# Performance work log

Measured on AMD Instinct MI355X. Metric: run time of the kernel, lower is better.

## Reference

```python
import jax, jax.numpy as jnp
import numpy as np

B, N, DIM = 16, 1024, 512
H, DH = 8, 64
INNER = H * DH            # 512
FF = 4 * DIM              # 2048
CIN = 2 * DIM             # conv inner dim = dim*expansion_factor = 1024
K = 31                    # depthwise kernel size
MAXPOS = 512
EPS = 1e-5


def layernorm(x, g, b):
    mu = jnp.mean(x, axis=-1, keepdims=True)
    var = jnp.mean(jnp.square(x - mu), axis=-1, keepdims=True)
    return (x - mu) * jax.lax.rsqrt(var + EPS) * g + b


def swish(x):
    return x * jax.nn.sigmoid(x)


def feed_forward(x, w1, b1, w2, b2):
    h = swish(x @ w1 + b1)
    return h @ w2 + b2


def setup_inputs() -> dict:
    key = jax.random.key(0)
    ks = jax.random.split(key, 16)
    s = 0.02
    w = lambda k, shape: (jax.random.normal(k, shape, jnp.float32) * s)
    inp = {
        "x": jax.random.normal(ks[0], (B, N, DIM), jnp.float32),
        # FF1
        "ff1_ln_g": jnp.ones((DIM,), jnp.float32), "ff1_ln_b": jnp.zeros((DIM,), jnp.float32),
        "ff1_w1": w(ks[1], (DIM, FF)), "ff1_b1": jnp.zeros((FF,), jnp.float32),
        "ff1_w2": w(ks[2], (FF, DIM)), "ff1_b2": jnp.zeros((DIM,), jnp.float32),
        # Attention (PreNorm)
        "attn_ln_g": jnp.ones((DIM,), jnp.float32), "attn_ln_b": jnp.zeros((DIM,), jnp.float32),
        "wq": w(ks[3], (DIM, INNER)),
        "wkv": w(ks[4], (DIM, 2 * INNER)),
        "wo": w(ks[5], (INNER, DIM)), "bo": jnp.zeros((DIM,), jnp.float32),
        "rel_emb": w(ks[6], (2 * MAXPOS + 1, DH)),
        # Conv module
        "conv_ln_g": jnp.ones((DIM,), jnp.float32), "conv_ln_b": jnp.zeros((DIM,), jnp.float32),
        "conv1_w": w(ks[7], (DIM, 2 * CIN)), "conv1_b": jnp.zeros((2 * CIN,), jnp.float32),
        "dw_w": w(ks[8], (CIN, 1, K)), "dw_b": jnp.zeros((CIN,), jnp.float32),
        "conv2_w": w(ks[9], (CIN, DIM)), "conv2_b": jnp.zeros((DIM,), jnp.float32),
        # FF2
        "ff2_ln_g": jnp.ones((DIM,), jnp.float32), "ff2_ln_b": jnp.zeros((DIM,), jnp.float32),
        "ff2_w1": w(ks[10], (DIM, FF)), "ff2_b1": jnp.zeros((FF,), jnp.float32),
        "ff2_w2": w(ks[11], (FF, DIM)), "ff2_b2": jnp.zeros((DIM,), jnp.float32),
        # post norm
        "post_ln_g": jnp.ones((DIM,), jnp.float32), "post_ln_b": jnp.zeros((DIM,), jnp.float32),
    }
    return inp


def attention(x, wq, wkv, wo, bo, rel_emb):
    b, n, _ = x.shape
    scale = DH ** -0.5
    q = (x @ wq).reshape(b, n, H, DH).transpose(0, 2, 1, 3)   # b h n d
    kv = x @ wkv
    k = kv[..., :INNER].reshape(b, n, H, DH).transpose(0, 2, 1, 3)
    v = kv[..., INNER:].reshape(b, n, H, DH).transpose(0, 2, 1, 3)
    dots = jnp.einsum("bhid,bhjd->bhij", q, k) * scale
    # relative positional bias via embedding lookup
    seq = jnp.arange(n)
    dist = jnp.clip(seq[:, None] - seq[None, :], -MAXPOS, MAXPOS) + MAXPOS  # [n, n]
    rel = jnp.take(rel_emb, dist, axis=0)                      # [n, n, d]
    pos = jnp.einsum("bhnd,njd->bhnj", q, rel) * scale
    attn = jax.nn.softmax(dots + pos, axis=-1)
    out = jnp.einsum("bhij,bhjd->bhid", attn, v)
    out = out.transpose(0, 2, 1, 3).reshape(b, n, INNER)
    return out @ wo + bo


def conv_module(x, ln_g, ln_b, conv1_w, conv1_b, dw_w, dw_b, conv2_w, conv2_b):
    h = layernorm(x, ln_g, ln_b)                               # [b, n, dim]
    h = h @ conv1_w + conv1_b                                  # pointwise conv -> [b, n, 2*CIN]
    a, g = h[..., :CIN], h[..., CIN:]
    h = a * jax.nn.sigmoid(g)                                  # GLU (channel dim)
    hc = h.transpose(0, 2, 1)                                  # [b, CIN, n]
    hc = jnp.pad(hc, ((0, 0), (0, 0), (K - 1, 0)))             # causal left pad
    hc = jax.lax.conv_general_dilated(
        hc, dw_w, window_strides=(1,), padding="VALID",
        feature_group_count=CIN, dimension_numbers=("NCH", "OIH", "NCH"),
    ) + dw_b[None, :, None]
    h = hc.transpose(0, 2, 1)                                  # [b, n, CIN]
    h = swish(h)
    return h @ conv2_w + conv2_b


def reference(x, ff1_ln_g, ff1_ln_b, ff1_w1, ff1_b1, ff1_w2, ff1_b2,
              attn_ln_g, attn_ln_b, wq, wkv, wo, bo, rel_emb,
              conv_ln_g, conv_ln_b, conv1_w, conv1_b, dw_w, dw_b, conv2_w, conv2_b,
              ff2_ln_g, ff2_ln_b, ff2_w1, ff2_b1, ff2_w2, ff2_b2,
              post_ln_g, post_ln_b):
    x = 0.5 * feed_forward(layernorm(x, ff1_ln_g, ff1_ln_b), ff1_w1, ff1_b1, ff1_w2, ff1_b2) + x
    x = attention(layernorm(x, attn_ln_g, attn_ln_b), wq, wkv, wo, bo, rel_emb) + x
    x = conv_module(x, conv_ln_g, conv_ln_b, conv1_w, conv1_b, dw_w, dw_b, conv2_w, conv2_b) + x
    x = 0.5 * feed_forward(layernorm(x, ff2_ln_g, ff2_ln_b), ff2_w1, ff2_b1, ff2_w2, ff2_b2) + x
    return layernorm(x, post_ln_g, post_ln_b)
```

## Files before the change

### kernel.cpp

```cpp
#include <hip/hip_runtime.h>


#define BN 16384

typedef unsigned short u16;
typedef __attribute__((ext_vector_type(8))) __bf16 bf16x8;
typedef __attribute__((ext_vector_type(4))) float f32x4;
typedef __attribute__((ext_vector_type(8))) unsigned short u16x8;

__device__ __forceinline__ float sigf(float x) { return 1.f / (1.f + __expf(-x)); }
__device__ __forceinline__ u16 f2bf(float f) {
  unsigned int u = __float_as_uint(f);
  u += 0x7FFF + ((u >> 16) & 1);
  return (u16)(u >> 16);
}
__device__ __forceinline__ float bf2f(u16 u) {
  return __uint_as_float(((unsigned int)u) << 16);
}
__device__ __forceinline__ void gl_lds16(const void* g, void* lds) {
  __builtin_amdgcn_global_load_lds(
      (const __attribute__((address_space(1))) unsigned int*)g,
      (__attribute__((address_space(3))) unsigned int*)lds, 16, 0, 0);
}

__global__ __launch_bounds__(256) void ln_kernel(const float* __restrict__ in,
    const float* __restrict__ g, const float* __restrict__ b,
    u16* outb, float* outf) {
  const int row = blockIdx.x;
  const int t = threadIdx.x;
  const float2 v = ((const float2*)(in + (size_t)row * 512))[t];
  float s = v.x + v.y;
  float sq = v.x * v.x + v.y * v.y;
#pragma unroll
  for (int o = 32; o > 0; o >>= 1) {
    s += __shfl_down(s, o);
    sq += __shfl_down(sq, o);
  }
  __shared__ float ss[4], ssq[4];
  if ((t & 63) == 0) { ss[t >> 6] = s; ssq[t >> 6] = sq; }
  __syncthreads();
  s = ss[0] + ss[1] + ss[2] + ss[3];
  sq = ssq[0] + ssq[1] + ssq[2] + ssq[3];
  const float mu = s * (1.f / 512.f);
  const float var = fmaxf(sq * (1.f / 512.f) - mu * mu, 0.f);
  const float rstd = rsqrtf(var + 1e-5f);
  const float2 gg = ((const float2*)g)[t];
  const float2 bb = ((const float2*)b)[t];
  float ox = (v.x - mu) * rstd * gg.x + bb.x;
  float oy = (v.y - mu) * rstd * gg.y + bb.y;
  if (outf) {
    float2 o2 = {ox, oy};
    ((float2*)(outf + (size_t)row * 512))[t] = o2;
  } else {
    ushort2 u2 = {f2bf(ox), f2bf(oy)};
    ((ushort2*)(outb + (size_t)row * 512))[t] = u2;
  }
}

__global__ __launch_bounds__(256) void wtrans(const float* __restrict__ W,
                                              u16* __restrict__ WT, int K, int N) {
  const int n0 = blockIdx.x * 32, k0 = blockIdx.y * 32;
  const int t = threadIdx.x;
  const int tx = t & 31, ty = t >> 5;
  __shared__ float T[32][33];
#pragma unroll
  for (int i = 0; i < 4; ++i)
    T[tx][ty + 8 * i] = W[(size_t)(k0 + ty + 8 * i) * N + n0 + tx];
  __syncthreads();
#pragma unroll
  for (int i = 0; i < 4; ++i)
    WT[(size_t)(n0 + ty + 8 * i) * K + k0 + tx] = f2bf(T[ty + 8 * i][tx]);
}

__global__ __launch_bounds__(256) void cvt_bf16(const float* __restrict__ in,
                                                u16* __restrict__ out, int n) {
  const int i = blockIdx.x * 256 + threadIdx.x;
  if (i < n) out[i] = f2bf(in[i]);
}

__global__ __launch_bounds__(256) void gemm_bf16(const u16* __restrict__ A,
    const u16* __restrict__ WT, const float* __restrict__ bias,
    const float* res, float* Cf, u16* Cb, u16* VTout, int K, int N, int ldc,
    float alpha, int act) {
  __shared__ __align__(16) u16 Ast[128 * 32];
  __shared__ __align__(16) u16 Bst[128 * 32];
  const int t = threadIdx.x;
  int bx = blockIdx.x, by = blockIdx.y;
  {
    const int nx = gridDim.x;
    const int lin = bx + nx * by;
    const int xcd = lin & 7;
    const int s = lin >> 3;
    const int ny8 = gridDim.y >> 3;
    const int sy = s / nx;
    by = xcd * ny8 + sy;
    bx = s - sy * nx;
  }
  const int n0 = bx * 128;
  const int m0 = by * 128;
  const int w = t >> 6;
  const int lc = t & 15, lq = (t >> 4) & 3;
  const int wy = w >> 1, wx = w & 1;
  f32x4 acc[4][4];
#pragma unroll
  for (int i = 0; i < 4; ++i)
#pragma unroll
    for (int j = 0; j < 4; ++j)
#pragma unroll
      for (int r = 0; r < 4; ++r) acc[i][j][r] = 0.f;

  for (int kt = 0; kt < K; kt += 32) {
#pragma unroll
    for (int s = 0; s < 2; ++s) {
      const int f = t + 256 * s;
      gl_lds16(&A[(size_t)(m0 + (f >> 2)) * K + kt + (f & 3) * 8], &Ast[f * 8]);
      gl_lds16(&WT[(size_t)(n0 + (f >> 2)) * K + kt + (f & 3) * 8], &Bst[f * 8]);
    }
    __syncthreads();
    bf16x8 bfr[4];
#pragma unroll
    for (int j = 0; j < 4; ++j)
      bfr[j] = *(const bf16x8*)&Bst[(wx * 64 + j * 16 + lc) * 32 + lq * 8];
#pragma unroll
    for (int i = 0; i < 4; ++i) {
      const bf16x8 af = *(const bf16x8*)&Ast[(wy * 64 + i * 16 + lc) * 32 + lq * 8];
#pragma unroll
      for (int j = 0; j < 4; ++j)
        acc[i][j] = __builtin_amdgcn_mfma_f32_16x16x32_bf16(af, bfr[j], acc[i][j], 0, 0, 0);
    }
    __syncthreads();
  }

#pragma unroll
  for (int j = 0; j < 4; ++j) {
    const int col = n0 + wx * 64 + j * 16 + lc;
    const float bj = bias ? bias[col] : 0.f;
    const bool vtc = (VTout != nullptr) && (col >= 512);
#pragma unroll
    for (int i = 0; i < 4; ++i) {
      const int row0 = m0 + wy * 64 + i * 16 + lq * 4;
      float v4[4];
#pragma unroll
      for (int r = 0; r < 4; ++r) {
        float v = acc[i][j][r] + bj;
        if (act) v = v * sigf(v);
        v *= alpha;
        if (res) v += res[(size_t)(row0 + r) * ldc + col];
        v4[r] = v;
      }
      if (vtc) {
        const int cm = col - 512;
        const int hh = cm >> 6, dd = cm & 63;
        const int bb = row0 >> 10, nl = row0 & 1023;
        ushort4 o4 = {f2bf(v4[0]), f2bf(v4[1]), f2bf(v4[2]), f2bf(v4[3])};
        *(ushort4*)&VTout[((size_t)((bb * 8 + hh) * 64 + dd)) * 1024 + nl] = o4;
      } else {
#pragma unroll
        for (int r = 0; r < 4; ++r) {
          const size_t off = (size_t)(row0 + r) * ldc + col;
          if (Cf) Cf[off] = v4[r];
          else Cb[off] = f2bf(v4[r]);
        }
      }
    }
  }
}

__global__ __launch_bounds__(256) void attn_mfma(const u16* __restrict__ QKV,
    const u16* __restrict__ Vt, const u16* __restrict__ Rb, u16* __restrict__ O) {
  const int lin = blockIdx.x;
  const int hb = lin & 127;
  const int n0 = (lin >> 7) * 64;
  const int h = hb & 7, b = hb >> 3;
  const int t = threadIdx.x;
  const int w = t >> 6;
  const int lc = t & 15, lq = (t >> 4) & 3;

  __shared__ __align__(16) u16 Ks[64 * 72];
  __shared__ __align__(16) u16 Vs[64 * 72];
  __shared__ __align__(16) u16 SP[64 * 72];

  bf16x8 qf[2];
  {
    const size_t qrow = (size_t)(b * 1024 + n0 + w * 16 + lc) * 1536 + h * 64;
    qf[0] = *(const bf16x8*)&QKV[qrow + lq * 8];
    qf[1] = *(const bf16x8*)&QKV[qrow + 32 + lq * 8];
  }

  float l_r[4] = {0.f, 0.f, 0.f, 0.f};
  f32x4 o[4];
#pragma unroll
  for (int dt = 0; dt < 4; ++dt)
#pragma unroll
    for (int r = 0; r < 4; ++r) o[dt][r] = 0.f;

  for (int jt = 0; jt < 16; ++jt) {
    const int j0 = jt * 64;
#pragma unroll
    for (int s = 0; s < 2; ++s) {
      const int f = t + 256 * s;
      const int row = f >> 3, c8 = (f & 7) * 8;
      const u16x8 kv =
          *(const u16x8*)&QKV[(size_t)(b * 1024 + j0 + row) * 1536 + 512 + h * 64 + c8];
      const u16x8 vv =
          *(const u16x8*)&Vt[(size_t)((b * 8 + h) * 64 + row) * 1024 + j0 + c8];
      *(u16x8*)&Ks[row * 72 + c8] = kv;
      *(u16x8*)&Vs[row * 72 + c8] = vv;
    }
    __syncthreads();

    f32x4 qk[4], pa[5];
#pragma unroll
    for (int j = 0; j < 4; ++j)
#pragma unroll
      for (int r = 0; r < 4; ++r) qk[j][r] = 0.f;
#pragma unroll
    for (int rtl = 0; rtl < 5; ++rtl)
#pragma unroll
      for (int r = 0; r < 4; ++r) pa[rtl][r] = 0.f;

    const int base = n0 - j0 - 63;
#pragma unroll
    for (int ks = 0; ks < 2; ++ks) {
      bf16x8 rfr[5];
#pragma unroll
      for (int rtl = 0; rtl < 5; ++rtl) {
        const int didx = (w + rtl) * 16 + lc;
        int p = base + didx;
        p = (p < -512 ? -512 : (p > 512 ? 512 : p)) + 512;
        rfr[rtl] = *(const bf16x8*)&Rb[(size_t)p * 64 + ks * 32 + lq * 8];
      }
#pragma unroll
      for (int j = 0; j < 4; ++j) {
        const bf16x8 bf = *(const bf16x8*)&Ks[(j * 16 + lc) * 72 + ks * 32 + lq * 8];
        qk[j] = __builtin_amdgcn_mfma_f32_16x16x32_bf16(qf[ks], bf, qk[j], 0, 0, 0);
      }
#pragma unroll
      for (int rtl = 0; rtl < 5; ++rtl)
        pa[rtl] = __builtin_amdgcn_mfma_f32_16x16x32_bf16(qf[ks], rfr[rtl], pa[rtl], 0, 0, 0);
    }

#pragma unroll
    for (int rtl = 0; rtl < 5; ++rtl) {
      const int didx = (w + rtl) * 16 + lc;
#pragma unroll
      for (int r = 0; r < 4; ++r) {
        const int qr = w * 16 + lq * 4 + r;
        const int jc = qr - didx + 63;
        if ((unsigned)jc < 64u) SP[qr * 72 + jc] = f2bf(pa[rtl][r]);
      }
    }

#pragma unroll
    for (int r = 0; r < 4; ++r) {
      const int qr = w * 16 + lq * 4 + r;
#pragma unroll
      for (int ti = 0; ti < 4; ++ti) {
        const int a = qr * 72 + ti * 16 + lc;
        const float e = exp2f(qk[ti][r] + bf2f(SP[a]));
        SP[a] = f2bf(e);
        l_r[r] += e;
      }
    }

#pragma unroll
    for (int ks = 0; ks < 2; ++ks) {
      const bf16x8 af = *(const bf16x8*)&SP[(w * 16 + lc) * 72 + ks * 32 + lq * 8];
#pragma unroll
      for (int dt = 0; dt < 4; ++dt) {
        const bf16x8 bf = *(const bf16x8*)&Vs[(dt * 16 + lc) * 72 + ks * 32 + lq * 8];
        o[dt] = __builtin_amdgcn_mfma_f32_16x16x32_bf16(af, bf, o[dt], 0, 0, 0);
      }
    }
    __syncthreads();
  }

#pragma unroll
  for (int r = 0; r < 4; ++r) {
#pragma unroll
    for (int msk = 1; msk < 16; msk <<= 1) l_r[r] += __shfl_xor(l_r[r], msk);
  }

#pragma unroll
  for (int r = 0; r < 4; ++r) {
    const float inv = 1.f / l_r[r];
    const size_t row = (size_t)(b * 1024 + n0 + w * 16 + lq * 4 + r);
#pragma unroll
    for (int dt = 0; dt < 4; ++dt)
      O[row * 512 + h * 64 + dt * 16 + lc] = f2bf(o[dt][r] * inv);
  }
}

__global__ __launch_bounds__(256) void glu_kernel(const u16* __restrict__ in,
                                                  u16* __restrict__ out) {
  const size_t m = blockIdx.x;
  const int c4 = threadIdx.x * 4;
  const ushort4 a4 = *(const ushort4*)&in[m * 2048 + c4];
  const ushort4 g4 = *(const ushort4*)&in[m * 2048 + 1024 + c4];
  ushort4 o4;
  o4.x = f2bf(bf2f(a4.x) * sigf(bf2f(g4.x)));
  o4.y = f2bf(bf2f(a4.y) * sigf(bf2f(g4.y)));
  o4.z = f2bf(bf2f(a4.z) * sigf(bf2f(g4.z)));
  o4.w = f2bf(bf2f(a4.w) * sigf(bf2f(g4.w)));
  *(ushort4*)&out[m * 1024 + c4] = o4;
}

__global__ __launch_bounds__(256) void dwconv_kernel(const u16* __restrict__ in,
    const float* __restrict__ w, const float* __restrict__ bias,
    u16* __restrict__ out) {
  const int n0 = blockIdx.x * 64;
  const int c0 = blockIdx.y * 64;
  const int b = blockIdx.z;
  const int t = threadIdx.x;
  __shared__ float hs[94][64];
  __shared__ float wsh[31][64];
  const int c = t & 63;
  const int g = t >> 6;
  for (int r = g; r < 94; r += 4) {
    const int n = n0 - 30 + r;
    hs[r][c] = (n >= 0) ? bf2f(in[(size_t)(b * 1024 + n) * 1024 + c0 + c]) : 0.f;
  }
  for (int idx = t; idx < 31 * 64; idx += 256) {
    const int tap = idx >> 6, cc = idx & 63;
    wsh[tap][cc] = w[(size_t)(c0 + cc) * 31 + tap];
  }
  __syncthreads();
  float wr[31];
#pragma unroll
  for (int k = 0; k < 31; ++k) wr[k] = wsh[k][c];
  const float bsv = bias[c0 + c];
  float win[46];
  const int rbase = g * 16;
#pragma unroll
  for (int k = 0; k < 46; ++k) win[k] = hs[rbase + k][c];
#pragma unroll
  for (int i = 0; i < 16; ++i) {
    float acc = bsv;
#pragma unroll
    for (int k = 0; k < 31; ++k) acc += wr[k] * win[i + k];
    acc = acc * sigf(acc);
    out[(size_t)(b * 1024 + n0 + rbase + i) * 1024 + c0 + c] = f2bf(acc);
  }
}

extern "C" void kernel_launch(void* const* d_in, const int* in_sizes, int n_in,
                              void* d_out, int out_size, void* d_ws, size_t ws_size,
                              hipStream_t stream) {
  const float* x        = (const float*)d_in[0];
  const float* ff1_ln_g = (const float*)d_in[1];
  const float* ff1_ln_b = (const float*)d_in[2];
  const float* ff1_w1   = (const float*)d_in[3];
  const float* ff1_b1   = (const float*)d_in[4];
  const float* ff1_w2   = (const float*)d_in[5];
  const float* ff1_b2   = (const float*)d_in[6];
  const float* attn_ln_g= (const float*)d_in[7];
  const float* attn_ln_b= (const float*)d_in[8];
  const float* wq       = (const float*)d_in[9];
  const float* wkv      = (const float*)d_in[10];
  const float* wo       = (const float*)d_in[11];
  const float* bo       = (const float*)d_in[12];
  const float* rel_emb  = (const float*)d_in[13];
  const float* conv_ln_g= (const float*)d_in[14];
  const float* conv_ln_b= (const float*)d_in[15];
  const float* conv1_w  = (const float*)d_in[16];
  const float* conv1_b  = (const float*)d_in[17];
  const float* dw_w     = (const float*)d_in[18];
  const float* dw_b     = (const float*)d_in[19];
  const float* conv2_w  = (const float*)d_in[20];
  const float* conv2_b  = (const float*)d_in[21];
  const float* ff2_ln_g = (const float*)d_in[22];
  const float* ff2_ln_b = (const float*)d_in[23];
  const float* ff2_w1   = (const float*)d_in[24];
  const float* ff2_b1   = (const float*)d_in[25];
  const float* ff2_w2   = (const float*)d_in[26];
  const float* ff2_b2   = (const float*)d_in[27];
  const float* post_ln_g= (const float*)d_in[28];
  const float* post_ln_b= (const float*)d_in[29];

  float* XRES = (float*)d_out;
  u16* ws = (u16*)d_ws;
  u16* LNB  = ws;
  u16* HID  = LNB + (size_t)BN * 512;
  u16* QKVB = HID + (size_t)BN * 2048;
  u16* VT   = QKVB + (size_t)BN * 1536;
  u16* GLUB = QKVB;
  u16* DWB  = HID;
  u16* WTp = VT + (size_t)8192 * 1024;
  u16* wt_ff1w1 = WTp;                 WTp += (size_t)2048 * 512;
  u16* wt_ff1w2 = WTp;                 WTp += (size_t)512 * 2048;
  u16* wt_qkv   = WTp;                 WTp += (size_t)1536 * 512;
  u16* wt_wo    = WTp;                 WTp += (size_t)512 * 512;
  u16* wt_conv1 = WTp;                 WTp += (size_t)2048 * 512;
  u16* wt_conv2 = WTp;                 WTp += (size_t)512 * 1024;
  u16* wt_ff2w1 = WTp;                 WTp += (size_t)2048 * 512;
  u16* wt_ff2w2 = WTp;                 WTp += (size_t)512 * 2048;
  u16* RELB     = WTp;

  const dim3 blk(256);
  const float SC = 0.125f * 1.44269504f;

  wtrans<<<dim3(64, 16), blk, 0, stream>>>(ff1_w1, wt_ff1w1, 512, 2048);
  wtrans<<<dim3(16, 64), blk, 0, stream>>>(ff1_w2, wt_ff1w2, 2048, 512);
  wtrans<<<dim3(16, 16), blk, 0, stream>>>(wq, wt_qkv, 512, 512);
  wtrans<<<dim3(32, 16), blk, 0, stream>>>(wkv, wt_qkv + (size_t)512 * 512, 512, 1024);
  wtrans<<<dim3(16, 16), blk, 0, stream>>>(wo, wt_wo, 512, 512);
  wtrans<<<dim3(64, 16), blk, 0, stream>>>(conv1_w, wt_conv1, 512, 2048);
  wtrans<<<dim3(16, 32), blk, 0, stream>>>(conv2_w, wt_conv2, 1024, 512);
  wtrans<<<dim3(64, 16), blk, 0, stream>>>(ff2_w1, wt_ff2w1, 512, 2048);
  wtrans<<<dim3(16, 64), blk, 0, stream>>>(ff2_w2, wt_ff2w2, 2048, 512);
  cvt_bf16<<<257, blk, 0, stream>>>(rel_emb, RELB, 1025 * 64);

  ln_kernel<<<BN, blk, 0, stream>>>(x, ff1_ln_g, ff1_ln_b, LNB, nullptr);
  gemm_bf16<<<dim3(16, 128), blk, 0, stream>>>(LNB, wt_ff1w1, ff1_b1, nullptr,
                                               nullptr, HID, nullptr, 512, 2048, 2048, 1.f, 1);
  gemm_bf16<<<dim3(4, 128), blk, 0, stream>>>(HID, wt_ff1w2, ff1_b2, x,
                                              XRES, nullptr, nullptr, 2048, 512, 512, 0.5f, 0);

  ln_kernel<<<BN, blk, 0, stream>>>(XRES, attn_ln_g, attn_ln_b, LNB, nullptr);
  gemm_bf16<<<dim3(4, 128), blk, 0, stream>>>(LNB, wt_qkv, nullptr, nullptr,
                                              nullptr, QKVB, nullptr, 512, 512, 1536, SC, 0);
  gemm_bf16<<<dim3(8, 128), blk, 0, stream>>>(LNB, wt_qkv + (size_t)512 * 512,
                                              nullptr, nullptr, nullptr, QKVB + 512,
                                              VT, 512, 1024, 1536, 1.f, 0);
  attn_mfma<<<dim3(2048), blk, 0, stream>>>(QKVB, VT, RELB, LNB);
  gemm_bf16<<<dim3(4, 128), blk, 0, stream>>>(LNB, wt_wo, bo, XRES,
                                              XRES, nullptr, nullptr, 512, 512, 512, 1.f, 0);

  ln_kernel<<<BN, blk, 0, stream>>>(XRES, conv_ln_g, conv_ln_b, LNB, nullptr);
  gemm_bf16<<<dim3(16, 128), blk, 0, stream>>>(LNB, wt_conv1, conv1_b, nullptr,
                                               nullptr, HID, nullptr, 512, 2048, 2048, 1.f, 0);
  glu_kernel<<<BN, blk, 0, stream>>>(HID, GLUB);
  dwconv_kernel<<<dim3(16, 16, 16), blk, 0, stream>>>(GLUB, dw_w, dw_b, DWB);
  gemm_bf16<<<dim3(4, 128), blk, 0, stream>>>(DWB, wt_conv2, conv2_b, XRES,
                                              XRES, nullptr, nullptr, 1024, 512, 512, 1.f, 0);

  ln_kernel<<<BN, blk, 0, stream>>>(XRES, ff2_ln_g, ff2_ln_b, LNB, nullptr);
  gemm_bf16<<<dim3(16, 128), blk, 0, stream>>>(LNB, wt_ff2w1, ff2_b1, nullptr,
                                               nullptr, HID, nullptr, 512, 2048, 2048, 1.f, 1);
  gemm_bf16<<<dim3(4, 128), blk, 0, stream>>>(HID, wt_ff2w2, ff2_b2, XRES,
                                              XRES, nullptr, nullptr, 2048, 512, 512, 0.5f, 0);

  ln_kernel<<<BN, blk, 0, stream>>>(XRES, post_ln_g, post_ln_b, nullptr, XRES);
}
```

Measured before the change: 966.0 us.

## Double-buffer attention K/V tiles with async global-to-LDS loads and XOR swizzle

The attention kernel now prefetches the next K/V tile straight into a second LDS buffer with global_load_lds while the current tile is being computed. This is meant to hide global memory latency behind the MFMA work. Padded LDS rows are replaced by an XOR-swizzled layout to avoid bank conflicts, and the trailing barrier per iteration is removed. Relative-embedding row pointers are also computed once per tile instead of once per k-step. Correctness now depends on the async loads being complete when the single barrier at the top of each iteration is reached.

```diff
diff --git a/kernel.cpp b/kernel.cpp
--- a/kernel.cpp
+++ b/kernel.cpp
@@ -176,8 +176,8 @@
   const int w = t >> 6;
   const int lc = t & 15, lq = (t >> 4) & 3;
 
-  __shared__ __align__(16) u16 Ks[64 * 72];
-  __shared__ __align__(16) u16 Vs[64 * 72];
+  __shared__ __align__(16) u16 Ks[2][64 * 64];
+  __shared__ __align__(16) u16 Vs[2][64 * 64];
   __shared__ __align__(16) u16 SP[64 * 72];
 
   bf16x8 qf[2];
@@ -187,6 +187,19 @@
     qf[1] = *(const bf16x8*)&QKV[qrow + 32 + lq * 8];
   }
 
+  const u16* Kg = QKV + (size_t)b * 1024 * 1536 + 512 + h * 64;
+  const u16* Vg = Vt + (size_t)(b * 8 + h) * 64 * 1024;
+
+  const int srow = t >> 3;
+  const int scb0 = ((t & 7) ^ (srow & 7)) * 8;
+  const int srow1 = (t + 256) >> 3;
+  const int scb1 = (((t + 256) & 7) ^ (srow1 & 7)) * 8;
+
+  gl_lds16(&Kg[(size_t)srow * 1536 + scb0], &Ks[0][t * 8]);
+  gl_lds16(&Vg[(size_t)srow * 1024 + scb0], &Vs[0][t * 8]);
+  gl_lds16(&Kg[(size_t)srow1 * 1536 + scb1], &Ks[0][(t + 256) * 8]);
+  gl_lds16(&Vg[(size_t)srow1 * 1024 + scb1], &Vs[0][(t + 256) * 8]);
+
   float l_r[4] = {0.f, 0.f, 0.f, 0.f};
   f32x4 o[4];
 #pragma unroll
@@ -194,21 +207,22 @@
 #pragma unroll
     for (int r = 0; r < 4; ++r) o[dt][r] = 0.f;
 
+  const int swz0 = (lq ^ (lc & 7)) * 8;
+  const int swz1 = ((4 + lq) ^ (lc & 7)) * 8;
+
+  int buf = 0;
   for (int jt = 0; jt < 16; ++jt) {
     const int j0 = jt * 64;
-#pragma unroll
-    for (int s = 0; s < 2; ++s) {
-      const int f = t + 256 * s;
-      const int row = f >> 3, c8 = (f & 7) * 8;
-      const u16x8 kv =
-          *(const u16x8*)&QKV[(size_t)(b * 1024 + j0 + row) * 1536 + 512 + h * 64 + c8];
-      const u16x8 vv =
-          *(const u16x8*)&Vt[(size_t)((b * 8 + h) * 64 + row) * 1024 + j0 + c8];
-      *(u16x8*)&Ks[row * 72 + c8] = kv;
-      *(u16x8*)&Vs[row * 72 + c8] = vv;
-    }
     __syncthreads();
 
+    if (jt < 15) {
+      const int j1 = j0 + 64;
+      gl_lds16(&Kg[(size_t)(j1 + srow) * 1536 + scb0], &Ks[buf ^ 1][t * 8]);
+      gl_lds16(&Vg[(size_t)srow * 1024 + j1 + scb0], &Vs[buf ^ 1][t * 8]);
+      gl_lds16(&Kg[(size_t)(j1 + srow1) * 1536 + scb1], &Ks[buf ^ 1][(t + 256) * 8]);
+      gl_lds16(&Vg[(size_t)srow1 * 1024 + j1 + scb1], &Vs[buf ^ 1][(t + 256) * 8]);
+    }
+
     f32x4 qk[4], pa[5];
 #pragma unroll
     for (int j = 0; j < 4; ++j)
@@ -220,19 +234,24 @@
       for (int r = 0; r < 4; ++r) pa[rtl][r] = 0.f;
 
     const int base = n0 - j0 - 63;
+    const u16* rp[5];
+#pragma unroll
+    for (int rtl = 0; rtl < 5; ++rtl) {
+      int p = base + (w + rtl) * 16 + lc;
+      p = (p < -512 ? -512 : (p > 512 ? 512 : p)) + 512;
+      rp[rtl] = Rb + (size_t)p * 64 + lq * 8;
+    }
+
 #pragma unroll
     for (int ks = 0; ks < 2; ++ks) {
+      const int koff = ks ? swz1 : swz0;
       bf16x8 rfr[5];
 #pragma unroll
-      for (int rtl = 0; rtl < 5; ++rtl) {
-        const int didx = (w + rtl) * 16 + lc;
-        int p = base + didx;
-        p = (p < -512 ? -512 : (p > 512 ? 512 : p)) + 512;
-        rfr[rtl] = *(const bf16x8*)&Rb[(size_t)p * 64 + ks * 32 + lq * 8];
-      }
+      for (int rtl = 0; rtl < 5; ++rtl)
+        rfr[rtl] = *(const bf16x8*)&rp[rtl][ks * 32];
 #pragma unroll
       for (int j = 0; j < 4; ++j) {
-        const bf16x8 bf = *(const bf16x8*)&Ks[(j * 16 + lc) * 72 + ks * 32 + lq * 8];
+        const bf16x8 bf = *(const bf16x8*)&Ks[buf][(j * 16 + lc) * 64 + koff];
         qk[j] = __builtin_amdgcn_mfma_f32_16x16x32_bf16(qf[ks], bf, qk[j], 0, 0, 0);
       }
 #pragma unroll
@@ -266,13 +285,14 @@
 #pragma unroll
     for (int ks = 0; ks < 2; ++ks) {
       const bf16x8 af = *(const bf16x8*)&SP[(w * 16 + lc) * 72 + ks * 32 + lq * 8];
+      const int koff = ks ? swz1 : swz0;
 #pragma unroll
       for (int dt = 0; dt < 4; ++dt) {
-        const bf16x8 bf = *(const bf16x8*)&Vs[(dt * 16 + lc) * 72 + ks * 32 + lq * 8];
+        const bf16x8 bf = *(const bf16x8*)&Vs[buf][(dt * 16 + lc) * 64 + koff];
         o[dt] = __builtin_amdgcn_mfma_f32_16x16x32_bf16(af, bf, o[dt], 0, 0, 0);
       }
     }
-    __syncthreads();
+    buf ^= 1;
   }
 
 #pragma unroll
```

New measurement: 956.8 us. Within noise of the previous version (-1.0%).
